# Optimization experiments

Hardware: AMD Instinct MI355X
Metric: run time of the kernel (lower is better)

Reference implementation:

```python
import jax, jax.numpy as jnp
import numpy as np

K = 5
PAD = K // 2
MARGIN = 0.3
EPS_AFF = 1e-9


def setup_inputs() -> dict:
    key = jax.random.key(0)
    k1, k2 = jax.random.split(key)
    pred = jax.random.normal(k1, (4, 64, 192, 640), dtype=jnp.float32)
    target = jax.random.randint(k2, (4, 1, 192, 640), 0, 20, dtype=jnp.int32)
    return {"pred": pred, "target": target}


def _loss_map(pred, target):
    # pred: [B,C,h,w] float, target: [B,1,h,w] int labels (same spatial size
    # as pred, so the nearest-neighbor interpolate in torch is the identity).
    B, C, h, w = pred.shape
    center = target  # [B,1,h,w]
    # label padding uses value=-1 (never matches a real label)
    pad_lbl = jnp.pad(center, ((0, 0), (0, 0), (PAD, PAD), (PAD, PAD)),
                      constant_values=-1)
    # F.normalize(feature, dim=1): x / max(||x||, 1e-12)
    norm = jnp.sqrt(jnp.sum(pred * pred, axis=1, keepdims=True))
    feat = pred / jnp.maximum(norm, 1e-12)
    pad_feat = jnp.pad(feat, ((0, 0), (0, 0), (PAD, PAD), (PAD, PAD)))

    labels, sims = [], []
    for i in range(K):          # fixed 5x5 window, 25 shifted slices
        for j in range(K):
            sh_lbl = pad_lbl[:, :, i:i + h, j:j + w]
            labels.append(center == sh_lbl)
            sh_feat = pad_feat[:, :, i:i + h, j:j + w]
            sims.append(jnp.sum(feat * sh_feat, axis=1, keepdims=True))
    agg = jnp.stack(labels, axis=-1).astype(jnp.float32)  # [B,1,h,w,25]
    sim = jnp.stack(sims, axis=-1)                          # [B,1,h,w,25]

    pos = agg
    neg = 1.0 - agg
    pos_num = jnp.sum(pos, axis=-1)   # [B,1,h,w]; >= 1 (center matches itself)
    neg_num = jnp.sum(neg, axis=-1)
    boundary = (pos_num >= K - 1) & (neg_num >= K - 1)

    affinity = jnp.sqrt(jnp.maximum(EPS_AFF, 2.0 - 2.0 * sim))  # [B,1,h,w,25]
    pos_dist = jnp.sum(pos * affinity, axis=-1) / pos_num
    neg_dist = jnp.sum(neg * affinity, axis=-1) / jnp.maximum(neg_num, 1e-12)

    triplet = jnp.maximum(0.0, pos_dist - neg_dist + MARGIN)
    # torch does boolean indexing loss_map = max(0, ...)[boundary]; we keep the
    # static-shape equivalent: full map zeroed outside the boundary region.
    return jnp.where(boundary, triplet, 0.0)


def reference(pred, target):
    return _loss_map(pred, target)
```

## Files before the change

### kernel.cpp

```cpp
#include <hip/hip_runtime.h>

constexpr int Bn = 4, Cn = 64, Hn = 192, Wn = 640, HW = Hn * Wn;
constexpr int TH = 8, TW = 64;
constexpr int SH = TH + 4, SW = TW + 4;
constexpr int NS = SH * SW;
constexpr int NT = 512;
constexpr int CH = 4;
constexpr int NCHUNK = Cn / CH;
constexpr int DR = SH - 2;
constexpr int ND = DR * SW;
constexpr int NPAIR = (DR / 2) * SW;
constexpr int ARENA = 12 * ND;

__global__ __launch_bounds__(NT, 4) void guide_triplet_kernel(
    const float* __restrict__ pred,
    const int*   __restrict__ target,
    float* __restrict__ out)
{
    __shared__ float arena[ARENA];
    __shared__ float invnS[NS];
    __shared__ int   lblS[NS];

    const int x0 = blockIdx.x * TW;
    const int y0 = blockIdx.y * TH;
    const int b  = blockIdx.z;

    const int tid = threadIdx.x;
    const int tx  = tid & (TW - 1);
    const int ty  = tid >> 6;

    const int e0 = tid;
    const int e1 = tid + NT;
    const bool has1 = (e1 < NS);
    const int r0 = e0 / SW, c0 = e0 % SW;
    const int r1 = e1 / SW, c1 = e1 % SW;
    const int gy0 = y0 + r0 - 2, gx0 = x0 + c0 - 2;
    const int gy1 = y0 + r1 - 2, gx1 = x0 + c1 - 2;
    const bool ok0 = (gy0 >= 0) && (gy0 < Hn) && (gx0 >= 0) && (gx0 < Wn);
    const bool ok1 = has1 && (gy1 >= 0) && (gy1 < Hn) && (gx1 >= 0) && (gx1 < Wn);
    const int off0 = gy0 * Wn + gx0;
    const int off1 = gy1 * Wn + gx1;

    {
        const int* tb = target + b * HW;
        lblS[e0] = ok0 ? tb[off0] : -1;
        if (has1) lblS[e1] = ok1 ? tb[off1] : -1;
    }

    const bool isPair = (tid < NPAIR);
    const int pa = tid / SW;
    const int pc = tid - pa * SW;
    const int rA = 2 * pa;

    float ss0 = 0.0f, ss1 = 0.0f;
    float accA[12], accB[12];
    #pragma unroll
    for (int i = 0; i < 12; ++i) { accA[i] = 0.0f; accB[i] = 0.0f; }

    const float* predb = pred + (size_t)b * Cn * HW;

    float ld0[CH], ld1[CH];
    #pragma unroll
    for (int cc = 0; cc < CH; ++cc) {
        ld0[cc] = ok0 ? predb[cc * HW + off0] : 0.0f;
        ld1[cc] = ok1 ? predb[cc * HW + off1] : 0.0f;
    }

    for (int chunk = 0; chunk < NCHUNK; ++chunk) {
        float* sb = arena + (chunk & 1) * (CH * NS);

        #pragma unroll
        for (int cc = 0; cc < CH; ++cc) {
            sb[cc * NS + e0] = ld0[cc];
            ss0 = fmaf(ld0[cc], ld0[cc], ss0);
            if (has1) {
                sb[cc * NS + e1] = ld1[cc];
                ss1 = fmaf(ld1[cc], ld1[cc], ss1);
            }
        }
        __syncthreads();

        if (chunk + 1 < NCHUNK) {
            const float* pc_ = predb + (size_t)(chunk + 1) * CH * HW;
            #pragma unroll
            for (int cc = 0; cc < CH; ++cc) {
                ld0[cc] = ok0 ? pc_[cc * HW + off0] : 0.0f;
                ld1[cc] = ok1 ? pc_[cc * HW + off1] : 0.0f;
            }
        }

        if (isPair) {
            #pragma unroll
            for (int cc = 0; cc < CH; ++cc) {
                const float* s0 = sb + cc * NS + rA * SW + pc;
                const float w00 = s0[0], w01 = s0[1], w02 = s0[2];
                const float* s1 = s0 + (SW - 2);
                const float w10 = s1[0], w11 = s1[1], w12 = s1[2],
                            w13 = s1[3], w14 = s1[4];
                const float* s2 = s1 + SW;
                const float w20 = s2[0], w21 = s2[1], w22 = s2[2],
                            w23 = s2[3], w24 = s2[4];
                const float* s3 = s2 + SW;
                const float w30 = s3[0], w31 = s3[1], w32 = s3[2],
                            w33 = s3[3], w34 = s3[4];
                accA[0]  = fmaf(w00, w01, accA[0]);
                accA[1]  = fmaf(w00, w02, accA[1]);
                accA[2]  = fmaf(w00, w10, accA[2]);
                accA[3]  = fmaf(w00, w11, accA[3]);
                accA[4]  = fmaf(w00, w12, accA[4]);
                accA[5]  = fmaf(w00, w13, accA[5]);
                accA[6]  = fmaf(w00, w14, accA[6]);
                accA[7]  = fmaf(w00, w20, accA[7]);
                accA[8]  = fmaf(w00, w21, accA[8]);
                accA[9]  = fmaf(w00, w22, accA[9]);
                accA[10] = fmaf(w00, w23, accA[10]);
                accA[11] = fmaf(w00, w24, accA[11]);
                accB[0]  = fmaf(w12, w13, accB[0]);
                accB[1]  = fmaf(w12, w14, accB[1]);
                accB[2]  = fmaf(w12, w20, accB[2]);
                accB[3]  = fmaf(w12, w21, accB[3]);
                accB[4]  = fmaf(w12, w22, accB[4]);
                accB[5]  = fmaf(w12, w23, accB[5]);
                accB[6]  = fmaf(w12, w24, accB[6]);
                accB[7]  = fmaf(w12, w30, accB[7]);
                accB[8]  = fmaf(w12, w31, accB[8]);
                accB[9]  = fmaf(w12, w32, accB[9]);
                accB[10] = fmaf(w12, w33, accB[10]);
                accB[11] = fmaf(w12, w34, accB[11]);
            }
        }
    }

    invnS[e0] = 1.0f / fmaxf(sqrtf(ss0), 1e-12f);
    if (has1) invnS[e1] = 1.0f / fmaxf(sqrtf(ss1), 1e-12f);
    __syncthreads();

    if (isPair) {
        const int qA = rA * SW + pc;
        const int qB = qA + SW;
        #pragma unroll
        for (int k = 0; k < 12; ++k) {
            arena[k * ND + qA] = accA[k];
            arena[k * ND + qB] = accB[k];
        }
    }
    __syncthreads();

    const int qp = (2 + ty) * SW + (2 + tx);
    const float ic = invnS[qp];
    const int   lc = lblS[qp];

    float pn = 1.0f, nn = 0.0f, ps = 3.16227766e-5f, ns_ = 0.0f;

    constexpr int DIRD[12] = {1, 2, SW - 2, SW - 1, SW, SW + 1, SW + 2,
                              2 * SW - 2, 2 * SW - 1, 2 * SW, 2 * SW + 1, 2 * SW + 2};
    #pragma unroll
    for (int k = 0; k < 12; ++k) {
        const int dq = DIRD[k];
        {
            const float sim = arena[k * ND + qp] * ic * invnS[qp + dq];
            const float aff = sqrtf(fmaxf(1e-9f, 2.0f - 2.0f * sim));
            const float mf  = (lblS[qp + dq] == lc) ? 1.0f : 0.0f;
            pn += mf; nn += 1.0f - mf;
            ps = fmaf(mf, aff, ps); ns_ = fmaf(1.0f - mf, aff, ns_);
        }
        {
            const float sim = arena[k * ND + qp - dq] * ic * invnS[qp - dq];
            const float aff = sqrtf(fmaxf(1e-9f, 2.0f - 2.0f * sim));
            const float mf  = (lblS[qp - dq] == lc) ? 1.0f : 0.0f;
            pn += mf; nn += 1.0f - mf;
            ps = fmaf(mf, aff, ps); ns_ = fmaf(1.0f - mf, aff, ns_);
        }
    }
    const bool boundary = (pn >= 4.0f) && (nn >= 4.0f);
    const float tri = fmaxf(0.0f, ps / pn - ns_ / fmaxf(nn, 1e-12f) + 0.3f);
    out[((size_t)b * Hn + (y0 + ty)) * Wn + (x0 + tx)] = boundary ? tri : 0.0f;
}

extern "C" void kernel_launch(void* const* d_in, const int* in_sizes, int n_in,
                              void* d_out, int out_size, void* d_ws, size_t ws_size,
                              hipStream_t stream) {
    const float* pred   = (const float*)d_in[0];
    const int*   target = (const int*)d_in[1];
    float*       out    = (float*)d_out;
    dim3 grid(Wn / TW, Hn / TH, Bn);
    guide_triplet_kernel<<<grid, NT, 0, stream>>>(pred, target, out);
}
```

Baseline: 71.78 us.

## Vectorize halo loads as float2, double chunk size, precompute affinities per pair

```diff
diff --git a/kernel.cpp b/kernel.cpp
--- a/kernel.cpp
+++ b/kernel.cpp
@@ -4,21 +4,23 @@
 constexpr int TH = 8, TW = 64;
 constexpr int SH = TH + 4, SW = TW + 4;
 constexpr int NS = SH * SW;
+constexpr int NP = NS / 2;
+constexpr int PPR = SW / 2;
 constexpr int NT = 512;
-constexpr int CH = 4;
+constexpr int CH = 8;
 constexpr int NCHUNK = Cn / CH;
 constexpr int DR = SH - 2;
 constexpr int ND = DR * SW;
 constexpr int NPAIR = (DR / 2) * SW;
-constexpr int ARENA = 12 * ND;
+constexpr int ARENA = 2 * CH * NS;
 
 __global__ __launch_bounds__(NT, 4) void guide_triplet_kernel(
     const float* __restrict__ pred,
     const int*   __restrict__ target,
     float* __restrict__ out)
 {
-    __shared__ float arena[ARENA];
-    __shared__ float invnS[NS];
+    __shared__ alignas(16) float arena[ARENA];
+    __shared__ float invnS[NS + 4];
     __shared__ int   lblS[NS];
 
     const int x0 = blockIdx.x * TW;
@@ -29,65 +31,66 @@
     const int tx  = tid & (TW - 1);
     const int ty  = tid >> 6;
 
-    const int e0 = tid;
-    const int e1 = tid + NT;
-    const bool has1 = (e1 < NS);
-    const int r0 = e0 / SW, c0 = e0 % SW;
-    const int r1 = e1 / SW, c1 = e1 % SW;
-    const int gy0 = y0 + r0 - 2, gx0 = x0 + c0 - 2;
-    const int gy1 = y0 + r1 - 2, gx1 = x0 + c1 - 2;
-    const bool ok0 = (gy0 >= 0) && (gy0 < Hn) && (gx0 >= 0) && (gx0 < Wn);
-    const bool ok1 = has1 && (gy1 >= 0) && (gy1 < Hn) && (gx1 >= 0) && (gx1 < Wn);
-    const int off0 = gy0 * Wn + gx0;
-    const int off1 = gy1 * Wn + gx1;
+    const bool hasS = (tid < NP);
+    const int srow = tid / PPR;
+    const int spc  = tid - srow * PPR;
+    const int gy = y0 + srow - 2;
+    const int gx = x0 + 2 * spc - 2;
+    const bool okS = hasS && (gy >= 0) && (gy < Hn) && (gx >= 0) && (gx + 1 < Wn);
+    const int goff = gy * Wn + gx;
+    const int sidx = 2 * tid;
 
-    {
-        const int* tb = target + b * HW;
-        lblS[e0] = ok0 ? tb[off0] : -1;
-        if (has1) lblS[e1] = ok1 ? tb[off1] : -1;
+    if (hasS) {
+        int lx = -1, ly = -1;
+        if (okS) {
+            const int2 L = *reinterpret_cast<const int2*>(target + b * HW + goff);
+            lx = L.x; ly = L.y;
+        }
+        lblS[sidx]     = lx;
+        lblS[sidx + 1] = ly;
     }
+    if (tid < 4) invnS[NS + tid] = 1.0f;
 
     const bool isPair = (tid < NPAIR);
     const int pa = tid / SW;
     const int pc = tid - pa * SW;
     const int rA = 2 * pa;
 
-    float ss0 = 0.0f, ss1 = 0.0f;
+    float ssx = 0.0f, ssy = 0.0f;
     float accA[12], accB[12];
     #pragma unroll
     for (int i = 0; i < 12; ++i) { accA[i] = 0.0f; accB[i] = 0.0f; }
 
     const float* predb = pred + (size_t)b * Cn * HW;
 
-    float ld0[CH], ld1[CH];
-    #pragma unroll
-    for (int cc = 0; cc < CH; ++cc) {
-        ld0[cc] = ok0 ? predb[cc * HW + off0] : 0.0f;
-        ld1[cc] = ok1 ? predb[cc * HW + off1] : 0.0f;
-    }
+    float2 ld[CH];
+
+#define LOADCHUNK(CHUNK) do {                                               \
+    _Pragma("unroll")                                                       \
+    for (int cc = 0; cc < CH; ++cc) {                                       \
+        const float* pc_ = predb + (size_t)((CHUNK) * CH + cc) * HW;        \
+        float2 v = make_float2(0.f, 0.f);                                   \
+        if (okS) v = *reinterpret_cast<const float2*>(pc_ + goff);          \
+        ld[cc] = v;                                                         \
+    } } while (0)
+
+    LOADCHUNK(0);
 
     for (int chunk = 0; chunk < NCHUNK; ++chunk) {
         float* sb = arena + (chunk & 1) * (CH * NS);
 
-        #pragma unroll
-        for (int cc = 0; cc < CH; ++cc) {
-            sb[cc * NS + e0] = ld0[cc];
-            ss0 = fmaf(ld0[cc], ld0[cc], ss0);
-            if (has1) {
-                sb[cc * NS + e1] = ld1[cc];
-                ss1 = fmaf(ld1[cc], ld1[cc], ss1);
+        if (hasS) {
+            #pragma unroll
+            for (int cc = 0; cc < CH; ++cc) {
+                const float2 v = ld[cc];
+                *reinterpret_cast<float2*>(&sb[cc * NS + sidx]) = v;
+                ssx = fmaf(v.x, v.x, ssx);
+                ssy = fmaf(v.y, v.y, ssy);
             }
         }
         __syncthreads();
 
-        if (chunk + 1 < NCHUNK) {
-            const float* pc_ = predb + (size_t)(chunk + 1) * CH * HW;
-            #pragma unroll
-            for (int cc = 0; cc < CH; ++cc) {
-                ld0[cc] = ok0 ? pc_[cc * HW + off0] : 0.0f;
-                ld1[cc] = ok1 ? pc_[cc * HW + off1] : 0.0f;
-            }
-        }
+        if (chunk + 1 < NCHUNK) LOADCHUNK(chunk + 1);
 
         if (isPair) {
             #pragma unroll
@@ -131,49 +134,53 @@
         }
     }
 
-    invnS[e0] = 1.0f / fmaxf(sqrtf(ss0), 1e-12f);
-    if (has1) invnS[e1] = 1.0f / fmaxf(sqrtf(ss1), 1e-12f);
+    if (hasS) {
+        invnS[sidx]     = 1.0f / fmaxf(sqrtf(ssx), 1e-12f);
+        invnS[sidx + 1] = 1.0f / fmaxf(sqrtf(ssy), 1e-12f);
+    }
     __syncthreads();
+
+    constexpr int DIRD[12] = {1, 2, SW - 2, SW - 1, SW, SW + 1, SW + 2,
+                              2 * SW - 2, 2 * SW - 1, 2 * SW, 2 * SW + 1, 2 * SW + 2};
 
     if (isPair) {
         const int qA = rA * SW + pc;
         const int qB = qA + SW;
+        const float icA = invnS[qA];
+        const float icB = invnS[qB];
         #pragma unroll
         for (int k = 0; k < 12; ++k) {
-            arena[k * ND + qA] = accA[k];
-            arena[k * ND + qB] = accB[k];
+            const int dq = DIRD[k];
+            const float simA = accA[k] * icA * invnS[qA + dq];
+            const float simB = accB[k] * icB * invnS[qB + dq];
+            arena[k * ND + qA] = sqrtf(fmaxf(1e-9f, fmaf(-2.0f, simA, 2.0f)));
+            arena[k * ND + qB] = sqrtf(fmaxf(1e-9f, fmaf(-2.0f, simB, 2.0f)));
         }
     }
     __syncthreads();
 
     const int qp = (2 + ty) * SW + (2 + tx);
-    const float ic = invnS[qp];
-    const int   lc = lblS[qp];
+    const int lc = lblS[qp];
 
-    float pn = 1.0f, nn = 0.0f, ps = 3.16227766e-5f, ns_ = 0.0f;
-
-    constexpr int DIRD[12] = {1, 2, SW - 2, SW - 1, SW, SW + 1, SW + 2,
-                              2 * SW - 2, 2 * SW - 1, 2 * SW, 2 * SW + 1, 2 * SW + 2};
+    float tot = 0.0f, ps = 0.0f, pn = 0.0f;
     #pragma unroll
     for (int k = 0; k < 12; ++k) {
         const int dq = DIRD[k];
-        {
-            const float sim = arena[k * ND + qp] * ic * invnS[qp + dq];
-            const float aff = sqrtf(fmaxf(1e-9f, 2.0f - 2.0f * sim));
-            const float mf  = (lblS[qp + dq] == lc) ? 1.0f : 0.0f;
-            pn += mf; nn += 1.0f - mf;
-            ps = fmaf(mf, aff, ps); ns_ = fmaf(1.0f - mf, aff, ns_);
-        }
-        {
-            const float sim = arena[k * ND + qp - dq] * ic * invnS[qp - dq];
-            const float aff = sqrtf(fmaxf(1e-9f, 2.0f - 2.0f * sim));
-            const float mf  = (lblS[qp - dq] == lc) ? 1.0f : 0.0f;
-            pn += mf; nn += 1.0f - mf;
-            ps = fmaf(mf, aff, ps); ns_ = fmaf(1.0f - mf, aff, ns_);
-        }
+        const float affF = arena[k * ND + qp];
+        const float affB = arena[k * ND + qp - dq];
+        const float mfF = (lblS[qp + dq] == lc) ? 1.0f : 0.0f;
+        const float mfB = (lblS[qp - dq] == lc) ? 1.0f : 0.0f;
+        tot += affF + affB;
+        pn += mfF + mfB;
+        ps = fmaf(mfF, affF, fmaf(mfB, affB, ps));
     }
-    const bool boundary = (pn >= 4.0f) && (nn >= 4.0f);
-    const float tri = fmaxf(0.0f, ps / pn - ns_ / fmaxf(nn, 1e-12f) + 0.3f);
+    const float pos_num = pn + 1.0f;
+    const float pos_sum = ps + 3.16227766e-5f;
+    const float neg_num = 24.0f - pn;
+    const float neg_sum = tot - ps;
+    const bool boundary = (pos_num >= 4.0f) && (neg_num >= 4.0f);
+    const float tri = fmaxf(0.0f,
+        pos_sum / pos_num - neg_sum / fmaxf(neg_num, 1e-12f) + 0.3f);
     out[((size_t)b * Hn + (y0 + ty)) * Wn + (x0 + tx)] = boundary ? tri : 0.0f;
 }
 
```

Measured after the change: 100.2 us. 39.6% more time.
